# Optimization experiments

Measured on AMD Instinct MI355X. Metric: run time of the kernel, lower is better.

Reference implementation:

```python
import jax, jax.numpy as jnp
import numpy as np

B, S, MEM, L, E, H = 8, 512, 512, 4, 512, 8
DH = E // H
OBS = 128
K = MEM + S


def setup_inputs() -> dict:
    key = jax.random.key(0)
    ks = jax.random.split(key, 16)
    def w(k, shape, s=0.02):
        return jax.random.normal(k, shape, jnp.float32) * s
    # causal-with-memory mask: query i may attend to kv positions j <= MEM + i
    mask = jnp.arange(K)[None, None, None, :] <= (MEM + jnp.arange(S))[None, None, :, None]
    return {
        "obs": w(ks[0], (B, S, OBS), 1.0),
        "memories": w(ks[1], (B, MEM, L, E), 1.0),
        "mask": mask,
        "W_enc": w(ks[2], (OBS, E)), "b_enc": jnp.zeros((E,), jnp.float32),
        "ln1_s": jnp.ones((L, E), jnp.float32), "ln1_b": jnp.zeros((L, E), jnp.float32),
        "Wq": w(ks[3], (L, E, H, DH)), "bq": jnp.zeros((L, H, DH), jnp.float32),
        "Wk": w(ks[4], (L, E, H, DH)), "bk": jnp.zeros((L, H, DH), jnp.float32),
        "Wv": w(ks[5], (L, E, H, DH)), "bv": jnp.zeros((L, H, DH), jnp.float32),
        "Wr": w(ks[6], (L, E, H, DH)),
        "u_bias": w(ks[7], (L, H, DH)), "v_bias": w(ks[8], (L, H, DH)),
        "Wo": w(ks[9], (L, H, DH, E)), "bo": jnp.zeros((L, E), jnp.float32),
        "ln2_s": jnp.ones((L, E), jnp.float32), "ln2_b": jnp.zeros((L, E), jnp.float32),
        "W1": w(ks[10], (L, E, E)), "b1": jnp.zeros((L, E), jnp.float32),
        "W2": w(ks[11], (L, E, E)), "b2": jnp.zeros((L, E), jnp.float32),
    }


def _ln(x, s, b, eps=1e-6):
    m = x.mean(-1, keepdims=True)
    v = ((x - m) ** 2).mean(-1, keepdims=True)
    return (x - m) * jax.lax.rsqrt(v + eps) * s + b


def _rel_shift(x):
    # Transformer-XL relative shift: [B,H,Q,Kk] -> shifted [B,H,Q,Kk]
    b, h, q, k = x.shape
    x = jnp.pad(x, ((0, 0), (0, 0), (0, 0), (1, 0)))
    return x.reshape(b, h, k + 1, q)[:, :, 1:, :].reshape(b, h, q, k)


def _forward(obs, memories, mask, W_enc, b_enc, ln1_s, ln1_b, Wq, bq, Wk, bk, Wv, bv,
             Wr, u_bias, v_bias, Wo, bo, ln2_s, ln2_b, W1, b1, W2, b2):
    x = obs @ W_enc + b_enc  # [B,S,E]
    klen = memories.shape[1] + x.shape[1]
    e = x.shape[-1]
    # PositionalEmbedding: pos_seq = [klen, klen-1, ..., 1]
    inv_freq = 1.0 / (10000.0 ** (jnp.arange(0, e, 2, dtype=jnp.float32) / e))
    sin_inp = jnp.outer(jnp.arange(klen, 0, -1, dtype=jnp.float32), inv_freq)
    pe = jnp.concatenate([jnp.sin(sin_inp), jnp.cos(sin_inp)], axis=-1)  # [K,E]
    scale = 1.0 / jnp.sqrt(jnp.asarray(Wq.shape[-1], jnp.float32))
    for i in range(Wq.shape[0]):
        mem_cat = jnp.concatenate([memories[:, :, i], x], axis=1)  # [B,K,E]
        vk = _ln(mem_cat, ln1_s[i], ln1_b[i])
        qn = _ln(x, ln1_s[i], ln1_b[i])
        q = jnp.einsum('bse,ehd->bshd', qn, Wq[i]) + bq[i]
        k = jnp.einsum('bke,ehd->bkhd', vk, Wk[i]) + bk[i]
        vv = jnp.einsum('bke,ehd->bkhd', vk, Wv[i]) + bv[i]
        r = jnp.einsum('ke,ehd->khd', pe, Wr[i])
        ac = jnp.einsum('bqhd,bkhd->bhqk', q + u_bias[i], k)     # content term
        bd = _rel_shift(jnp.einsum('bqhd,khd->bhqk', q + v_bias[i], r))  # position term
        scores = jnp.where(mask, (ac + bd) * scale, jnp.float32(-1e30))
        attn = jax.nn.softmax(scores, axis=-1)
        o = jnp.einsum('bhqk,bkhd->bqhd', attn, vv)
        attn_out = jnp.einsum('bqhd,hde->bqe', o, Wo[i]) + bo[i]
        h = x + attn_out                      # residual (gating=False)
        hn = _ln(h, ln2_s[i], ln2_b[i])
        ff = jax.nn.gelu(hn @ W1[i] + b1[i]) @ W2[i] + b2[i]
        x = ff + h
    return x


def reference(obs, memories, mask, W_enc, b_enc, ln1_s, ln1_b, Wq, bq, Wk, bk, Wv, bv,
              Wr, u_bias, v_bias, Wo, bo, ln2_s, ln2_b, W1, b1, W2, b2):
    return _forward(obs, memories, mask, W_enc, b_enc, ln1_s, ln1_b, Wq, bq, Wk, bk,
                    Wv, bv, Wr, u_bias, v_bias, Wo, bo, ln2_s, ln2_b, W1, b1, W2, b2)
```

## Files before the change

kernel.cpp:

```cpp
#include <hip/hip_runtime.h>
#include <hip/hip_bf16.h>
#include <math.h>

#define B     8
#define S     512
#define MEM   512
#define L     4
#define E     512
#define H     8
#define DH    64
#define OBS   128
#define KLEN  1024
#define FQ    64
#define FK    64

typedef __hip_bfloat16 bf16;
using frag_ab = __attribute__((ext_vector_type(8))) short;
using frag_cd = __attribute__((ext_vector_type(4))) float;

__device__ __forceinline__ float gelu_tanh(float x) {
    return 0.5f * x * (1.0f + tanhf(0.7978845608028654f * (x + 0.044715f * x * x * x)));
}
__device__ __forceinline__ unsigned short f2bs(float x) {
    bf16 h = __float2bfloat16(x); return *(unsigned short*)&h;
}
__device__ __forceinline__ float bs2f(short s) {
    union { unsigned u; float f; } t; t.u = ((unsigned)(unsigned short)s) << 16; return t.f;
}

__global__ __launch_bounds__(256) void setup_kernel(
    const float* __restrict__ obs, bf16* __restrict__ obsb, bf16* __restrict__ pe)
{
    const int i = blockIdx.x * 256 + threadIdx.x;
    if (i < B * S * OBS) {
        obsb[i] = __float2bfloat16(obs[i]);
    } else {
        const int idx = i - B * S * OBS;
        const int p = idx >> 9;
        const int j = idx & 511;
        const float pos = (float)(KLEN - p);
        const int m = (j < 256) ? j : (j - 256);
        const float invf = expf(-(float)(2 * m) * (9.210340371976184f / (float)E));
        const float a = pos * invf;
        pe[idx] = __float2bfloat16((j < 256) ? sinf(a) : cosf(a));
    }
}

__global__ __launch_bounds__(256) void transpose_all_kernel(
    const float* __restrict__ Wq, const float* __restrict__ Wk,
    const float* __restrict__ Wv, const float* __restrict__ Wr,
    const float* __restrict__ Wo, const float* __restrict__ W1,
    const float* __restrict__ W2, const float* __restrict__ Wenc,
    bf16* __restrict__ WqT, bf16* __restrict__ WkvT, bf16* __restrict__ WrT,
    bf16* __restrict__ WoT, bf16* __restrict__ W1T, bf16* __restrict__ W2T,
    bf16* __restrict__ WencT)
{
    __shared__ float t[32][33];
    const int z = blockIdx.z;
    const int bn = blockIdx.x * 32, bk = blockIdx.y * 32;
    const int tx = threadIdx.x & 31, ty = threadIdx.x >> 5;
    if (z == 28) {
        if (blockIdx.y >= OBS / 32) return;
        #pragma unroll
        for (int r = 0; r < 32; r += 8)
            t[ty + r][tx] = Wenc[(size_t)(bk + ty + r) * E + bn + tx];
        __syncthreads();
        #pragma unroll
        for (int r = 0; r < 32; r += 8)
            WencT[(size_t)(bn + ty + r) * OBS + bk + tx] = __float2bfloat16(t[tx][ty + r]);
        return;
    }
    const int which = z >> 2, li = z & 3;
    const size_t so = (size_t)li * E * E;
    const float* src; bf16* dst;
    switch (which) {
        case 0: src = Wq + so; dst = WqT + so; break;
        case 1: src = Wk + so; dst = WkvT + (size_t)li * 2 * E * E; break;
        case 2: src = Wv + so; dst = WkvT + (size_t)li * 2 * E * E + (size_t)E * E; break;
        case 3: src = Wr + so; dst = WrT + so; break;
        case 4: src = Wo + so; dst = WoT + so; break;
        case 5: src = W1 + so; dst = W1T + so; break;
        default: src = W2 + so; dst = W2T + so; break;
    }
    #pragma unroll
    for (int r = 0; r < 32; r += 8)
        t[ty + r][tx] = src[(size_t)(bk + ty + r) * E + bn + tx];
    __syncthreads();
    #pragma unroll
    for (int r = 0; r < 32; r += 8)
        dst[(size_t)(bn + ty + r) * E + bk + tx] = __float2bfloat16(t[tx][ty + r]);
}

__global__ __launch_bounds__(256) void transpose_v_kernel(
    const bf16* __restrict__ Vn, bf16* __restrict__ Vt)
{
    __shared__ short ts[64][72];
    const int k0 = blockIdx.x * 64, d0 = blockIdx.y * 64, b = blockIdx.z;
    const int t = threadIdx.x;
    const int r = t >> 2, c = (t & 3) * 16;
    const short* src = (const short*)Vn + ((size_t)(b * KLEN + k0 + r)) * E + d0 + c;
    *(uint4*)&ts[r][c]     = *(const uint4*)(src);
    *(uint4*)&ts[r][c + 8] = *(const uint4*)(src + 8);
    __syncthreads();
    short vals[16];
    #pragma unroll
    for (int i = 0; i < 16; ++i) {
        const int kp = c + i;
        const int ks = ((kp & 3) << 4) | (kp >> 2);
        vals[i] = ts[ks][r];
    }
    short* dst = (short*)Vt + ((size_t)(b * E + d0 + r)) * KLEN + k0 + c;
    *(uint4*)(dst)     = *(const uint4*)&vals[0];
    *(uint4*)(dst + 8) = *(const uint4*)&vals[8];
}

__device__ __forceinline__ void gemm_body(
    short* As, short* Bs,
    const bf16* __restrict__ A, const bf16* __restrict__ Bt,
    int m0, int n0, int K, int N,
    const float* bias, const float* bias_u, const float* bias_v,
    const float* res, float* Cf, bf16* Cb, bf16* Cb2, int act, int mode)
{
    const int tid = threadIdx.x;
    const int w = tid >> 6, lane = tid & 63;
    const int wm2 = (w >> 1) * 64, wn2 = (w & 1) * 32;
    const int fr = lane & 15, quad = lane >> 4;

    const int arow = tid >> 1, acol = (tid & 1) * 32;
    const int brow = tid >> 2, bcol = (tid & 3) * 16;
    const short* Ag = (const short*)A + (size_t)(m0 + arow) * K + acol;
    const short* Bg = (const short*)Bt + (size_t)(n0 + brow) * K + bcol;
    short* Asw = &As[arow * 72 + acol];
    short* Bsw = &Bs[brow * 72 + bcol];

    frag_cd acc[4][2];
    #pragma unroll
    for (int i = 0; i < 4; ++i)
        #pragma unroll
        for (int j = 0; j < 2; ++j)
            acc[i][j] = (frag_cd)(0.0f);

    uint4 a0 = *(const uint4*)(Ag);
    uint4 a1 = *(const uint4*)(Ag + 8);
    uint4 a2 = *(const uint4*)(Ag + 16);
    uint4 a3 = *(const uint4*)(Ag + 24);
    uint4 b0 = *(const uint4*)(Bg);
    uint4 b1 = *(const uint4*)(Bg + 8);

    for (int k0 = 0; k0 < K; k0 += 64) {
        __syncthreads();
        *(uint4*)(Asw) = a0; *(uint4*)(Asw + 8) = a1;
        *(uint4*)(Asw + 16) = a2; *(uint4*)(Asw + 24) = a3;
        *(uint4*)(Bsw) = b0; *(uint4*)(Bsw + 8) = b1;
        if (k0 + 64 < K) {
            a0 = *(const uint4*)(Ag + k0 + 64);
            a1 = *(const uint4*)(Ag + k0 + 72);
            a2 = *(const uint4*)(Ag + k0 + 80);
            a3 = *(const uint4*)(Ag + k0 + 88);
            b0 = *(const uint4*)(Bg + k0 + 64);
            b1 = *(const uint4*)(Bg + k0 + 72);
        }
        asm volatile("s_waitcnt lgkmcnt(0)" ::: "memory");
        __builtin_amdgcn_s_barrier();
        __builtin_amdgcn_sched_barrier(0);
        #pragma unroll
        for (int kh = 0; kh < 2; ++kh) {
            frag_ab af[4], bfr[2];
            #pragma unroll
            for (int i = 0; i < 4; ++i)
                af[i] = *(const frag_ab*)&As[(wm2 + i * 16 + fr) * 72 + kh * 32 + quad * 8];
            #pragma unroll
            for (int j = 0; j < 2; ++j)
                bfr[j] = *(const frag_ab*)&Bs[(wn2 + j * 16 + fr) * 72 + kh * 32 + quad * 8];
            #pragma unroll
            for (int i = 0; i < 4; ++i)
                #pragma unroll
                for (int j = 0; j < 2; ++j)
                    acc[i][j] = __builtin_amdgcn_mfma_f32_16x16x32_bf16(af[i], bfr[j], acc[i][j], 0, 0, 0);
        }
    }

    #pragma unroll
    for (int i = 0; i < 4; ++i) {
        #pragma unroll
        for (int r = 0; r < 4; ++r) {
            const int m = m0 + wm2 + i * 16 + quad * 4 + r;
            #pragma unroll
            for (int j = 0; j < 2; ++j) {
                const int n = n0 + wn2 + j * 16 + fr;
                float v = acc[i][j][r];
                if (bias) v += bias[n];
                if (act)  v = gelu_tanh(v);
                if (res)  v += res[(size_t)m * N + n];
                if (mode == 2) {
                    if (n < 512) Cb[(size_t)m * 512 + n] = __float2bfloat16(v + bias_u[n]);
                    else Cb2[(size_t)m * 512 + (n - 512)] = __float2bfloat16(v + bias_v[n - 512]);
                } else if (mode == 1) {
                    Cb[(size_t)m * N + n]  = __float2bfloat16((v + bias_u[n]) * 0.125f);
                    Cb2[(size_t)m * N + n] = __float2bfloat16((v + bias_v[n]) * 0.125f);
                } else {
                    if (Cf) Cf[(size_t)m * N + n] = v;
                    if (Cb) Cb[(size_t)m * N + n] = __float2bfloat16(v);
                }
            }
        }
    }
}

__global__ __launch_bounds__(256) void mfma_gemm_kernel(
    const bf16* __restrict__ A, const bf16* __restrict__ Bt,
    const float* __restrict__ bias, const float* __restrict__ res,
    float* __restrict__ Cf, bf16* __restrict__ Cb,
    int K, int N, int act)
{
    __shared__ short As[128 * 72];
    __shared__ short Bs[64 * 72];
    const int pid = blockIdx.x;
    const int swz = ((pid & 7) << 5) | (pid >> 3);
    const int mblk = swz >> 3, nblk = swz & 7;
    gemm_body(As, Bs, A, Bt, mblk * 128, nblk * 64, K, N,
              bias, nullptr, nullptr, res, Cf, Cb, nullptr, act, 0);
}

__global__ __launch_bounds__(256) void qkvr_kernel(
    const bf16* __restrict__ QN, const bf16* __restrict__ VK,
    const bf16* __restrict__ PE_, const bf16* __restrict__ WqT,
    const bf16* __restrict__ WkvT, const bf16* __restrict__ WrT,
    const float* __restrict__ bq, const float* __restrict__ ub,
    const float* __restrict__ vbias, const float* __restrict__ bk,
    const float* __restrict__ bv,
    bf16* __restrict__ QU, bf16* __restrict__ QV,
    bf16* __restrict__ KB, bf16* __restrict__ VB, bf16* __restrict__ RB)
{
    __shared__ short As[128 * 72];
    __shared__ short Bs[64 * 72];
    const int bid = blockIdx.x;
    if (bid < 256) {
        const int swz = ((bid & 7) << 5) | (bid >> 3);
        gemm_body(As, Bs, QN, WqT, (swz >> 3) * 128, (swz & 7) * 64, E, E,
                  bq, ub, vbias, nullptr, nullptr, QU, QV, 0, 1);
    } else if (bid < 1280) {
        const int id = bid - 256;
        const int swz = ((id & 7) << 7) | (id >> 3);
        gemm_body(As, Bs, VK, WkvT, (swz >> 4) * 128, (swz & 15) * 64, E, 2 * E,
                  nullptr, bk, bv, nullptr, nullptr, KB, VB, 0, 2);
    } else {
        const int id = bid - 1280;
        const int swz = ((id & 7) << 3) | (id >> 3);
        gemm_body(As, Bs, PE_, WrT, (swz >> 3) * 128, (swz & 7) * 64, E, E,
                  nullptr, nullptr, nullptr, nullptr, nullptr, RB, nullptr, 0, 0);
    }
}

__global__ __launch_bounds__(256) void ln1_kernel(
    const float* __restrict__ mem, const float* __restrict__ X, int li,
    const float* __restrict__ gam, const float* __restrict__ bet,
    bf16* __restrict__ qn, bf16* __restrict__ vkdst)
{
    const int blk = blockIdx.x;
    const int t = threadIdx.x;
    const bool isMem = blk < B * MEM;
    const int rr = isMem ? blk : (blk - B * MEM);
    const float* sp = isMem ? (mem + ((size_t)rr * L + li) * E)
                            : (X + (size_t)rr * E);
    const float x0 = sp[t], x1 = sp[t + 256];
    float s = x0 + x1, ss = fmaf(x0, x0, x1 * x1);
    #pragma unroll
    for (int off = 32; off; off >>= 1) { s += __shfl_down(s, off, 64); ss += __shfl_down(ss, off, 64); }
    __shared__ float tmp[8];
    const int wid = t >> 6, lane = t & 63;
    if (!lane) { tmp[wid] = s; tmp[4 + wid] = ss; }
    __syncthreads();
    s = tmp[0] + tmp[1] + tmp[2] + tmp[3];
    ss = tmp[4] + tmp[5] + tmp[6] + tmp[7];
    const float mean = s * (1.0f / E);
    const float var = ss * (1.0f / E) - mean * mean;
    const float rstd = rsqrtf(var + 1e-6f);
    const float y0 = (x0 - mean) * rstd * gam[t] + bet[t];
    const float y1 = (x1 - mean) * rstd * gam[t + 256] + bet[t + 256];
    const int b = rr >> 9, p = rr & 511;
    if (isMem) {
        bf16* dst = vkdst + ((size_t)b * KLEN + p) * E;
        dst[t] = __float2bfloat16(y0); dst[t + 256] = __float2bfloat16(y1);
    } else {
        qn[(size_t)rr * E + t]       = __float2bfloat16(y0);
        qn[(size_t)rr * E + t + 256] = __float2bfloat16(y1);
        bf16* d2 = vkdst + ((size_t)b * KLEN + MEM + p) * E;
        d2[t] = __float2bfloat16(y0); d2[t + 256] = __float2bfloat16(y1);
    }
}

__global__ __launch_bounds__(256) void ln_f32_kernel(
    const float* __restrict__ src,
    const float* __restrict__ gam, const float* __restrict__ bet,
    bf16* __restrict__ dst1)
{
    const int rr = blockIdx.x;
    const int t = threadIdx.x;
    const float* sp = src + (size_t)rr * E;
    const float x0 = sp[t], x1 = sp[t + 256];
    float s = x0 + x1, ss = fmaf(x0, x0, x1 * x1);
    #pragma unroll
    for (int off = 32; off; off >>= 1) { s += __shfl_down(s, off, 64); ss += __shfl_down(ss, off, 64); }
    __shared__ float tmp[8];
    const int wid = t >> 6, lane = t & 63;
    if (!lane) { tmp[wid] = s; tmp[4 + wid] = ss; }
    __syncthreads();
    s = tmp[0] + tmp[1] + tmp[2] + tmp[3];
    ss = tmp[4] + tmp[5] + tmp[6] + tmp[7];
    const float mean = s * (1.0f / E);
    const float var = ss * (1.0f / E) - mean * mean;
    const float rstd = rsqrtf(var + 1e-6f);
    dst1[(size_t)rr * E + t]       = __float2bfloat16((x0 - mean) * rstd * gam[t] + bet[t]);
    dst1[(size_t)rr * E + t + 256] = __float2bfloat16((x1 - mean) * rstd * gam[t + 256] + bet[t + 256]);
}

__global__ __launch_bounds__(256) void mfma_flash_kernel(
    const bf16* __restrict__ Qu,
    const bf16* __restrict__ Qv,
    const bf16* __restrict__ Kb,
    const bf16* __restrict__ Vt,
    const bf16* __restrict__ Rb,
    bf16* __restrict__ O)
{
    const int pid = blockIdx.x;
    const int swz = ((pid & 7) << 6) | (pid >> 3);
    const int qphys = swz & 7;
    const int hb = swz >> 3;
    const int h = hb & 7, b = hb >> 3;
    const int qt = (qphys & 1) ? (7 - (qphys >> 1)) : (qphys >> 1);
    const int q0 = qt * FQ;
    const int t = threadIdx.x;
    const int w = t >> 6, lane = t & 63;
    const int fr = lane & 15, quad = lane >> 4;
    const int qbase = q0 + w * 16;

    __shared__ short Ks[64 * 64];
    __shared__ short Vs[64 * 64];
    __shared__ short Rs[128 * 64];
    __shared__ short BDs[4 * 80 * 18];
    __shared__ short Ps[4 * 16 * 64];

    const int fxk = fr & 7;
    const int xq0 = (quad ^ fxk) << 3;
    const int xq1 = ((quad + 4) ^ fxk) << 3;

    const short* quptr = (const short*)Qu + ((size_t)(b * S + qbase + fr)) * E + h * DH + quad * 8;
    const frag_ab au0 = *(const frag_ab*)(quptr);
    const frag_ab au1 = *(const frag_ab*)(quptr + 32);
    const short* qvptr = (const short*)Qv + ((size_t)(b * S + qbase + fr)) * E + h * DH + quad * 8;
    const frag_ab av0 = *(const frag_ab*)(qvptr);
    const frag_ab av1 = *(const frag_ab*)(qvptr + 32);

    frag_cd accO[4];
    #pragma unroll
    for (int i = 0; i < 4; ++i) accO[i] = (frag_cd)(0.0f);
    float mrow[4] = {-3.0e38f, -3.0e38f, -3.0e38f, -3.0e38f};
    float lrow[4] = {0.f, 0.f, 0.f, 0.f};

    const int srow = t >> 2, scol = (t & 3) * 16;
    const short* kg = (const short*)Kb + ((size_t)(b * KLEN + srow)) * E + h * DH + scol;
    const short* vg = (const short*)Vt + ((size_t)(b * E + h * DH + srow)) * KLEN + scol;
    const int sxs = srow & 7;
    const int scb = (t & 3) * 2;
    const int kvw0 = (srow << 6) + (((scb    ) ^ sxs) << 3);
    const int kvw1 = (srow << 6) + (((scb + 1) ^ sxs) << 3);
    const int ntb0 = 3 - w;
    const int b0 = 448 - q0;

    {
        const int rr = t >> 1, rc = (t & 1) * 32;
        const int j = b0 + rr;
        const int slot = j & 127;
        const int sx = slot & 7, cb = rc >> 3;
        const short* rp = (const short*)Rb + (size_t)j * E + h * DH + rc;
        *(uint4*)&Rs[(slot << 6) + (((cb    ) ^ sx) << 3)] = *(const uint4*)(rp);
        *(uint4*)&Rs[(slot << 6) + (((cb + 1) ^ sx) << 3)] = *(const uint4*)(rp + 8);
        *(uint4*)&Rs[(slot << 6) + (((cb + 2) ^ sx) << 3)] = *(const uint4*)(rp + 16);
        *(uint4*)&Rs[(slot << 6) + (((cb + 3) ^ sx) << 3)] = *(const uint4*)(rp + 24);
    }

    const int ntiles = 9 + qt;

    const int r64 = t >> 2, rc4 = (t & 3) * 16;
    uint4 ka0, ka1, va0, va1, ra0, ra1;
    int rslot = 0;
    {
        ka0 = *(const uint4*)(kg);
        ka1 = *(const uint4*)(kg + 8);
        va0 = *(const uint4*)(vg);
        va1 = *(const uint4*)(vg + 8);
    }

    for (int kt = 0; kt < ntiles; ++kt) {
        const int k0 = kt * FK;
        __syncthreads();
        {
            *(uint4*)&Ks[kvw0] = ka0;
            *(uint4*)&Ks[kvw1] = ka1;
            *(uint4*)&Vs[kvw0] = va0;
            *(uint4*)&Vs[kvw1] = va1;
        }
        if (kt >= 1) {
            const int sx = rslot & 7;
            *(uint4*)&Rs[(rslot << 6) + (((scb    ) ^ sx) << 3)] = ra0;
            *(uint4*)&Rs[(rslot << 6) + (((scb + 1) ^ sx) << 3)] = ra1;
        }
        if (kt + 1 < ntiles) {
            const short* kp = kg + (size_t)(k0 + FK) * E;
            ka0 = *(const uint4*)(kp);
            ka1 = *(const uint4*)(kp + 8);
            const short* vp = vg + k0 + FK;
            va0 = *(const uint4*)(vp);
            va1 = *(const uint4*)(vp + 8);
            int j = b0 + 64 * (kt + 1) + 64 + r64;
            rslot = j & 127;
            if (j > KLEN - 1) j = KLEN - 1;
            const short* rp = (const short*)Rb + (size_t)j * E + h * DH + rc4;
            ra0 = *(const uint4*)(rp);
            ra1 = *(const uint4*)(rp + 8);
        }
        asm volatile("s_waitcnt lgkmcnt(0)" ::: "memory");
        __builtin_amdgcn_s_barrier();
        __builtin_amdgcn_sched_barrier(0);

        const int roff = (b0 + 64 * kt) & 127;

        __builtin_amdgcn_s_setprio(1);
        #pragma unroll
        for (int i = 0; i < 5; ++i) {
            const int ntb = ntb0 + i;
            const int slot = (roff + ntb * 16 + fr) & 127;
            const frag_ab rf0 = *(const frag_ab*)&Rs[(slot << 6) + xq0];
            const frag_ab rf1 = *(const frag_ab*)&Rs[(slot << 6) + xq1];
            frag_cd z = (frag_cd)(0.0f);
            z = __builtin_amdgcn_mfma_f32_16x16x32_bf16(av0, rf0, z, 0, 0, 0);
            z = __builtin_amdgcn_mfma_f32_16x16x32_bf16(av1, rf1, z, 0, 0, 0);
            union { unsigned u[2]; unsigned short sh[4]; } pk;
            pk.sh[0] = f2bs(z[0]); pk.sh[1] = f2bs(z[1]);
            pk.sh[2] = f2bs(z[2]); pk.sh[3] = f2bs(z[3]);
            const int bdw = (w * 80 + i * 16 + fr) * 18 + quad * 4;
            *(unsigned*)&BDs[bdw]     = pk.u[0];
            *(unsigned*)&BDs[bdw + 2] = pk.u[1];
        }

        frag_cd sc[4];
        #pragma unroll
        for (int nt = 0; nt < 4; ++nt) {
            const int krow = (nt * 16 + fr) << 6;
            const frag_ab kf0 = *(const frag_ab*)&Ks[krow + xq0];
            const frag_ab kf1 = *(const frag_ab*)&Ks[krow + xq1];
            frag_cd z = (frag_cd)(0.0f);
            z = __builtin_amdgcn_mfma_f32_16x16x32_bf16(au0, kf0, z, 0, 0, 0);
            z = __builtin_amdgcn_mfma_f32_16x16x32_bf16(au1, kf1, z, 0, 0, 0);
            sc[nt] = z;
        }
        __builtin_amdgcn_s_setprio(0);

        const bool edge = (kt == ntiles - 1);
        #pragma unroll
        for (int r = 0; r < 4; ++r) {
            const int qw = quad * 4 + r;
            float sv[4];
            #pragma unroll
            for (int nt = 0; nt < 4; ++nt) {
                const int jlr = nt * 16 + fr + 15 - qw;
                const float bd = bs2f(BDs[(w * 80 + jlr) * 18 + qw]);
                sv[nt] = sc[nt][r] + bd;
            }
            if (edge) {
                const int qrow = qbase + qw;
                #pragma unroll
                for (int nt = 0; nt < 4; ++nt)
                    if (k0 + nt * 16 + fr > MEM + qrow) sv[nt] = -1e30f;
            }
            const float locmax = fmaxf(fmaxf(sv[0], sv[1]), fmaxf(sv[2], sv[3]));
            if (__any(locmax > mrow[r] + 4.0f)) {
                float tm = locmax;
                tm = fmaxf(tm, __shfl_xor(tm, 1, 64));
                tm = fmaxf(tm, __shfl_xor(tm, 2, 64));
                tm = fmaxf(tm, __shfl_xor(tm, 4, 64));
                tm = fmaxf(tm, __shfl_xor(tm, 8, 64));
                const float mn = fmaxf(mrow[r], tm);
                const float al = __expf(mrow[r] - mn);
                lrow[r] *= al;
                #pragma unroll
                for (int nt = 0; nt < 4; ++nt) accO[nt][r] *= al;
                mrow[r] = mn;
            }
            const float p0 = __expf(sv[0] - mrow[r]), p1 = __expf(sv[1] - mrow[r]);
            const float p2 = __expf(sv[2] - mrow[r]), p3 = __expf(sv[3] - mrow[r]);
            lrow[r] += (p0 + p1) + (p2 + p3);
            union { uint2 u2; unsigned short sh[4]; } pq;
            pq.sh[0] = f2bs(p0); pq.sh[1] = f2bs(p1);
            pq.sh[2] = f2bs(p2); pq.sh[3] = f2bs(p3);
            const int pw = (w << 10) + (qw << 6)
                         + (((fr >> 1) ^ (qw & 7)) << 3) + ((fr & 1) << 2);
            *(uint2*)&Ps[pw] = pq.u2;
        }

        const frag_ab pf0 = *(const frag_ab*)&Ps[(w << 10) + (fr << 6) + xq0];
        const frag_ab pf1 = *(const frag_ab*)&Ps[(w << 10) + (fr << 6) + xq1];
        __builtin_amdgcn_s_setprio(1);
        #pragma unroll
        for (int nt = 0; nt < 4; ++nt) {
            const int vrow = (nt * 16 + fr) << 6;
            const frag_ab vf0 = *(const frag_ab*)&Vs[vrow + xq0];
            const frag_ab vf1 = *(const frag_ab*)&Vs[vrow + xq1];
            accO[nt] = __builtin_amdgcn_mfma_f32_16x16x32_bf16(pf0, vf0, accO[nt], 0, 0, 0);
            accO[nt] = __builtin_amdgcn_mfma_f32_16x16x32_bf16(pf1, vf1, accO[nt], 0, 0, 0);
        }
        __builtin_amdgcn_s_setprio(0);
    }

    #pragma unroll
    for (int r = 0; r < 4; ++r) {
        float lsum = lrow[r];
        lsum += __shfl_xor(lsum, 1, 64);
        lsum += __shfl_xor(lsum, 2, 64);
        lsum += __shfl_xor(lsum, 4, 64);
        lsum += __shfl_xor(lsum, 8, 64);
        const float inv = 1.0f / lsum;
        bf16* po = O + ((size_t)(b * S + qbase + quad * 4 + r)) * E + h * DH + fr;
        #pragma unroll
        for (int nt = 0; nt < 4; ++nt)
            po[nt * 16] = __float2bfloat16(accO[nt][r] * inv);
    }
}

extern "C" void kernel_launch(void* const* d_in, const int* in_sizes, int n_in,
                              void* d_out, int out_size, void* d_ws, size_t ws_size,
                              hipStream_t stream)
{
    const float* obs  = (const float*)d_in[0];
    const float* mem  = (const float*)d_in[1];
    const float* Wenc = (const float*)d_in[3];
    const float* benc = (const float*)d_in[4];
    const float* ln1s = (const float*)d_in[5];
    const float* ln1b = (const float*)d_in[6];
    const float* Wq   = (const float*)d_in[7];
    const float* bq   = (const float*)d_in[8];
    const float* Wk   = (const float*)d_in[9];
    const float* bk   = (const float*)d_in[10];
    const float* Wv   = (const float*)d_in[11];
    const float* bv   = (const float*)d_in[12];
    const float* Wr   = (const float*)d_in[13];
    const float* ub   = (const float*)d_in[14];
    const float* vb   = (const float*)d_in[15];
    const float* Wo   = (const float*)d_in[16];
    const float* bo   = (const float*)d_in[17];
    const float* ln2s = (const float*)d_in[18];
    const float* ln2b = (const float*)d_in[19];
    const float* W1   = (const float*)d_in[20];
    const float* b1   = (const float*)d_in[21];
    const float* W2   = (const float*)d_in[22];
    const float* b2   = (const float*)d_in[23];

    float* wsf = (float*)d_ws;
    float* X = wsf;
    bf16* wsb = (bf16*)(wsf + (size_t)B * S * E);
    size_t ob = 0;
    bf16* OBSb = wsb + ob; ob += (size_t)B * S * OBS;
    bf16* QNb  = wsb + ob; ob += (size_t)B * S * E;
    bf16* PEb  = wsb + ob; ob += (size_t)KLEN * E;
    bf16* RBb  = wsb + ob; ob += (size_t)KLEN * E;
    bf16* WencT= wsb + ob; ob += (size_t)OBS * E;
    bf16* WqT  = wsb + ob; ob += (size_t)L * E * E;
    bf16* WkvT = wsb + ob; ob += (size_t)L * 2 * E * E;
    bf16* WrT  = wsb + ob; ob += (size_t)L * E * E;
    bf16* WoT  = wsb + ob; ob += (size_t)L * E * E;
    bf16* W1T  = wsb + ob; ob += (size_t)L * E * E;
    bf16* W2T  = wsb + ob; ob += (size_t)L * E * E;
    bf16* QUb  = wsb + ob; ob += (size_t)B * S * E;
    bf16* QVb  = wsb + ob; ob += (size_t)B * S * E;
    bf16* KBb  = wsb + ob; ob += (size_t)B * KLEN * E;
    bf16* VTb  = wsb + ob; ob += (size_t)B * E * KLEN;
    bf16* OBb  = wsb + ob; ob += (size_t)B * S * E;
    char* uni = (char*)(wsb + ob);
    bf16*  VKb = (bf16*)uni;
    bf16*  VBb = (bf16*)(uni + ((size_t)8 << 20));
    float* HB  = (float*)uni;
    bf16*  FFb = (bf16*)(uni + ((size_t)8 << 20));

    transpose_all_kernel<<<dim3(E / 32, E / 32, 29), 256, 0, stream>>>(
        Wq, Wk, Wv, Wr, Wo, W1, W2, Wenc, WqT, WkvT, WrT, WoT, W1T, W2T, WencT);
    setup_kernel<<<(B * S * OBS + KLEN * E) / 256, 256, 0, stream>>>(obs, OBSb, PEb);

    mfma_gemm_kernel<<<256, 256, 0, stream>>>(
        OBSb, WencT, benc, nullptr, X, nullptr, OBS, E, 0);

    for (int li = 0; li < L; ++li) {
        const size_t wOff = (size_t)li * E * E;
        const size_t vOff = (size_t)li * E;

        ln1_kernel<<<2 * B * S, 256, 0, stream>>>(
            mem, X, li, ln1s + vOff, ln1b + vOff, QNb, VKb);

        qkvr_kernel<<<1344, 256, 0, stream>>>(
            QNb, VKb, PEb, WqT + wOff, WkvT + (size_t)li * 2 * E * E, WrT + wOff,
            bq + vOff, ub + vOff, vb + vOff, bk + vOff, bv + vOff,
            QUb, QVb, KBb, VBb, RBb);

        transpose_v_kernel<<<dim3(KLEN / 64, E / 64, B), 256, 0, stream>>>(VBb, VTb);

        mfma_flash_kernel<<<512, 256, 0, stream>>>(
            QUb, QVb, KBb, VTb, RBb, OBb);

        mfma_gemm_kernel<<<256, 256, 0, stream>>>(
            OBb, WoT + wOff, bo + vOff, X, HB, nullptr, E, E, 0);
        ln_f32_kernel<<<B * S, 256, 0, stream>>>(HB, ln2s + vOff, ln2b + vOff, QNb);
        mfma_gemm_kernel<<<256, 256, 0, stream>>>(
            QNb, W1T + wOff, b1 + vOff, nullptr, nullptr, FFb, E, E, 1);
        mfma_gemm_kernel<<<256, 256, 0, stream>>>(
            FFb, W2T + wOff, b2 + vOff, HB, X, nullptr, E, E, 0);
    }

    hipMemcpyAsync(d_out, X, (size_t)B * S * E * sizeof(float),
                   hipMemcpyDeviceToDevice, stream);
}
```

Measured before the change: 702.6 us.

## Use direct global-to-LDS loads with XOR swizzle and double buffering in GEMM

Replaces the register-staged tile loads in the shared GEMM body with global_load_lds direct-to-LDS transfers into double-buffered shared tiles. Padding is replaced by an XOR swizzle to avoid bank conflicts. The next tile is prefetched while the current one is computed. This removes the register round trip and one barrier per iteration, at the cost of double the LDS footprint, which may lower occupancy.

```diff
diff --git a/kernel.cpp b/kernel.cpp
--- a/kernel.cpp
+++ b/kernel.cpp
@@ -26,6 +26,11 @@
 }
 __device__ __forceinline__ float bs2f(short s) {
     union { unsigned u; float f; } t; t.u = ((unsigned)(unsigned short)s) << 16; return t.f;
+}
+__device__ __forceinline__ void gload16(const short* g, short* l) {
+    __builtin_amdgcn_global_load_lds(
+        (const __attribute__((address_space(1))) void*)g,
+        (__attribute__((address_space(3))) void*)l, 16, 0, 0);
 }
 
 __global__ __launch_bounds__(256) void setup_kernel(
@@ -125,13 +130,16 @@
     const int w = tid >> 6, lane = tid & 63;
     const int wm2 = (w >> 1) * 64, wn2 = (w & 1) * 32;
     const int fr = lane & 15, quad = lane >> 4;
-
-    const int arow = tid >> 1, acol = (tid & 1) * 32;
-    const int brow = tid >> 2, bcol = (tid & 3) * 16;
-    const short* Ag = (const short*)A + (size_t)(m0 + arow) * K + acol;
-    const short* Bg = (const short*)Bt + (size_t)(n0 + brow) * K + bcol;
-    short* Asw = &As[arow * 72 + acol];
-    short* Bsw = &Bs[brow * 72 + bcol];
+    const int l3 = lane >> 3, l7 = lane & 7;
+    const int gch = (l7 ^ l3) * 8;
+
+    const size_t Kz = (size_t)K;
+    const short* Ag0 = (const short*)A + (size_t)(m0 + w * 32 + l3) * Kz + gch;
+    const short* Bg0 = (const short*)Bt + (size_t)(n0 + w * 16 + l3) * Kz + gch;
+
+    const int fx = fr & 7;
+    const int xq0 = (quad ^ fx) << 3;
+    const int xq1 = ((quad + 4) ^ fx) << 3;
 
     frag_cd acc[4][2];
     #pragma unroll
@@ -140,38 +148,42 @@
         for (int j = 0; j < 2; ++j)
             acc[i][j] = (frag_cd)(0.0f);
 
-    uint4 a0 = *(const uint4*)(Ag);
-    uint4 a1 = *(const uint4*)(Ag + 8);
-    uint4 a2 = *(const uint4*)(Ag + 16);
-    uint4 a3 = *(const uint4*)(Ag + 24);
-    uint4 b0 = *(const uint4*)(Bg);
-    uint4 b1 = *(const uint4*)(Bg + 8);
-
-    for (int k0 = 0; k0 < K; k0 += 64) {
-        __syncthreads();
-        *(uint4*)(Asw) = a0; *(uint4*)(Asw + 8) = a1;
-        *(uint4*)(Asw + 16) = a2; *(uint4*)(Asw + 24) = a3;
-        *(uint4*)(Bsw) = b0; *(uint4*)(Bsw + 8) = b1;
-        if (k0 + 64 < K) {
-            a0 = *(const uint4*)(Ag + k0 + 64);
-            a1 = *(const uint4*)(Ag + k0 + 72);
-            a2 = *(const uint4*)(Ag + k0 + 80);
-            a3 = *(const uint4*)(Ag + k0 + 88);
-            b0 = *(const uint4*)(Bg + k0 + 64);
-            b1 = *(const uint4*)(Bg + k0 + 72);
-        }
-        asm volatile("s_waitcnt lgkmcnt(0)" ::: "memory");
+    #pragma unroll
+    for (int i = 0; i < 4; ++i)
+        gload16(Ag0 + (size_t)(i * 8) * Kz, As + w * 2048 + i * 512);
+    #pragma unroll
+    for (int i = 0; i < 2; ++i)
+        gload16(Bg0 + (size_t)(i * 8) * Kz, Bs + w * 1024 + i * 512);
+
+    const int T = K >> 6;
+    for (int t = 0; t < T; ++t) {
+        const int cur = t & 1;
+        asm volatile("s_waitcnt vmcnt(0)" ::: "memory");
         __builtin_amdgcn_s_barrier();
         __builtin_amdgcn_sched_barrier(0);
+        if (t + 1 < T) {
+            const int nb = cur ^ 1;
+            const int k0 = (t + 1) << 6;
+            #pragma unroll
+            for (int i = 0; i < 4; ++i)
+                gload16(Ag0 + (size_t)(i * 8) * Kz + k0, As + nb * 8192 + w * 2048 + i * 512);
+            #pragma unroll
+            for (int i = 0; i < 2; ++i)
+                gload16(Bg0 + (size_t)(i * 8) * Kz + k0, Bs + nb * 4096 + w * 1024 + i * 512);
+        }
+        __builtin_amdgcn_sched_barrier(0);
+        const short* Ab = As + cur * 8192;
+        const short* Bb = Bs + cur * 4096;
         #pragma unroll
         for (int kh = 0; kh < 2; ++kh) {
+            const int xq = kh ? xq1 : xq0;
             frag_ab af[4], bfr[2];
             #pragma unroll
             for (int i = 0; i < 4; ++i)
-                af[i] = *(const frag_ab*)&As[(wm2 + i * 16 + fr) * 72 + kh * 32 + quad * 8];
+                af[i] = *(const frag_ab*)&Ab[(wm2 + i * 16 + fr) * 64 + xq];
             #pragma unroll
             for (int j = 0; j < 2; ++j)
-                bfr[j] = *(const frag_ab*)&Bs[(wn2 + j * 16 + fr) * 72 + kh * 32 + quad * 8];
+                bfr[j] = *(const frag_ab*)&Bb[(wn2 + j * 16 + fr) * 64 + xq];
             #pragma unroll
             for (int i = 0; i < 4; ++i)
                 #pragma unroll
@@ -213,8 +225,8 @@
     float* __restrict__ Cf, bf16* __restrict__ Cb,
     int K, int N, int act)
 {
-    __shared__ short As[128 * 72];
-    __shared__ short Bs[64 * 72];
+    __shared__ short As[2 * 128 * 64];
+    __shared__ short Bs[2 * 64 * 64];
     const int pid = blockIdx.x;
     const int swz = ((pid & 7) << 5) | (pid >> 3);
     const int mblk = swz >> 3, nblk = swz & 7;
@@ -232,8 +244,8 @@
     bf16* __restrict__ QU, bf16* __restrict__ QV,
     bf16* __restrict__ KB, bf16* __restrict__ VB, bf16* __restrict__ RB)
 {
-    __shared__ short As[128 * 72];
-    __shared__ short Bs[64 * 72];
+    __shared__ short As[2 * 128 * 64];
+    __shared__ short Bs[2 * 64 * 64];
     const int bid = blockIdx.x;
     if (bid < 256) {
         const int swz = ((bid & 7) << 5) | (bid >> 3);
```

Measured after the change: 724.8 us. +3.2%, slower.

## Use 64x64 GEMM tiles with 512 blocks and write final output directly

Applied to the files above, without the earlier changes.

Replaces the 128x64-tile GEMM body used by the dense projection GEMMs with a new 64x64-tile body, doubling the grid to 512 blocks. The goal is better CU occupancy on a 4096x512 problem, since 256 blocks underfill the device. The last layer's W2 GEMM now writes straight into the output buffer, which drops the final device-to-device memcpy. Smaller tiles lower data reuse per block and raise global load traffic.

```diff
diff --git a/kernel.cpp b/kernel.cpp
--- a/kernel.cpp
+++ b/kernel.cpp
@@ -207,19 +207,96 @@
     }
 }
 
+__device__ __forceinline__ void gemm64_body(
+    short* As, short* Bs,
+    const bf16* __restrict__ A, const bf16* __restrict__ Bt,
+    int m0, int n0, int K, int N,
+    const float* bias, const float* res, float* Cf, bf16* Cb, int act)
+{
+    const int tid = threadIdx.x;
+    const int w = tid >> 6, lane = tid & 63;
+    const int wm2 = (w >> 1) * 32, wn2 = (w & 1) * 32;
+    const int fr = lane & 15, quad = lane >> 4;
+
+    const int arow = tid >> 2, acol = (tid & 3) * 16;
+    const short* Ag = (const short*)A + (size_t)(m0 + arow) * K + acol;
+    const short* Bg = (const short*)Bt + (size_t)(n0 + arow) * K + acol;
+    short* Asw = &As[arow * 72 + acol];
+    short* Bsw = &Bs[arow * 72 + acol];
+
+    frag_cd acc[2][2];
+    #pragma unroll
+    for (int i = 0; i < 2; ++i)
+        #pragma unroll
+        for (int j = 0; j < 2; ++j)
+            acc[i][j] = (frag_cd)(0.0f);
+
+    uint4 a0 = *(const uint4*)(Ag);
+    uint4 a1 = *(const uint4*)(Ag + 8);
+    uint4 b0 = *(const uint4*)(Bg);
+    uint4 b1 = *(const uint4*)(Bg + 8);
+
+    for (int k0 = 0; k0 < K; k0 += 64) {
+        __syncthreads();
+        *(uint4*)(Asw) = a0; *(uint4*)(Asw + 8) = a1;
+        *(uint4*)(Bsw) = b0; *(uint4*)(Bsw + 8) = b1;
+        if (k0 + 64 < K) {
+            a0 = *(const uint4*)(Ag + k0 + 64);
+            a1 = *(const uint4*)(Ag + k0 + 72);
+            b0 = *(const uint4*)(Bg + k0 + 64);
+            b1 = *(const uint4*)(Bg + k0 + 72);
+        }
+        asm volatile("s_waitcnt lgkmcnt(0)" ::: "memory");
+        __builtin_amdgcn_s_barrier();
+        __builtin_amdgcn_sched_barrier(0);
+        #pragma unroll
+        for (int kh = 0; kh < 2; ++kh) {
+            frag_ab af[2], bfr[2];
+            #pragma unroll
+            for (int i = 0; i < 2; ++i)
+                af[i] = *(const frag_ab*)&As[(wm2 + i * 16 + fr) * 72 + kh * 32 + quad * 8];
+            #pragma unroll
+            for (int j = 0; j < 2; ++j)
+                bfr[j] = *(const frag_ab*)&Bs[(wn2 + j * 16 + fr) * 72 + kh * 32 + quad * 8];
+            #pragma unroll
+            for (int i = 0; i < 2; ++i)
+                #pragma unroll
+                for (int j = 0; j < 2; ++j)
+                    acc[i][j] = __builtin_amdgcn_mfma_f32_16x16x32_bf16(af[i], bfr[j], acc[i][j], 0, 0, 0);
+        }
+    }
+
+    #pragma unroll
+    for (int i = 0; i < 2; ++i) {
+        #pragma unroll
+        for (int r = 0; r < 4; ++r) {
+            const int m = m0 + wm2 + i * 16 + quad * 4 + r;
+            #pragma unroll
+            for (int j = 0; j < 2; ++j) {
+                const int n = n0 + wn2 + j * 16 + fr;
+                float v = acc[i][j][r];
+                if (bias) v += bias[n];
+                if (act)  v = gelu_tanh(v);
+                if (res)  v += res[(size_t)m * N + n];
+                if (Cf) Cf[(size_t)m * N + n] = v;
+                if (Cb) Cb[(size_t)m * N + n] = __float2bfloat16(v);
+            }
+        }
+    }
+}
+
 __global__ __launch_bounds__(256) void mfma_gemm_kernel(
     const bf16* __restrict__ A, const bf16* __restrict__ Bt,
     const float* __restrict__ bias, const float* __restrict__ res,
     float* __restrict__ Cf, bf16* __restrict__ Cb,
     int K, int N, int act)
 {
-    __shared__ short As[128 * 72];
+    __shared__ short As[64 * 72];
     __shared__ short Bs[64 * 72];
     const int pid = blockIdx.x;
-    const int swz = ((pid & 7) << 5) | (pid >> 3);
-    const int mblk = swz >> 3, nblk = swz & 7;
-    gemm_body(As, Bs, A, Bt, mblk * 128, nblk * 64, K, N,
-              bias, nullptr, nullptr, res, Cf, Cb, nullptr, act, 0);
+    const int swz = ((pid & 7) << 6) | (pid >> 3);
+    gemm64_body(As, Bs, A, Bt, (swz >> 3) * 64, (swz & 7) * 64, K, N,
+                bias, res, Cf, Cb, act);
 }
 
 __global__ __launch_bounds__(256) void qkvr_kernel(
@@ -586,7 +663,7 @@
         Wq, Wk, Wv, Wr, Wo, W1, W2, Wenc, WqT, WkvT, WrT, WoT, W1T, W2T, WencT);
     setup_kernel<<<(B * S * OBS + KLEN * E) / 256, 256, 0, stream>>>(obs, OBSb, PEb);
 
-    mfma_gemm_kernel<<<256, 256, 0, stream>>>(
+    mfma_gemm_kernel<<<512, 256, 0, stream>>>(
         OBSb, WencT, benc, nullptr, X, nullptr, OBS, E, 0);
 
     for (int li = 0; li < L; ++li) {
@@ -606,15 +683,13 @@
         mfma_flash_kernel<<<512, 256, 0, stream>>>(
             QUb, QVb, KBb, VTb, RBb, OBb);
 
-        mfma_gemm_kernel<<<256, 256, 0, stream>>>(
+        mfma_gemm_kernel<<<512, 256, 0, stream>>>(
             OBb, WoT + wOff, bo + vOff, X, HB, nullptr, E, E, 0);
         ln_f32_kernel<<<B * S, 256, 0, stream>>>(HB, ln2s + vOff, ln2b + vOff, QNb);
-        mfma_gemm_kernel<<<256, 256, 0, stream>>>(
+        mfma_gemm_kernel<<<512, 256, 0, stream>>>(
             QNb, W1T + wOff, b1 + vOff, nullptr, nullptr, FFb, E, E, 1);
-        mfma_gemm_kernel<<<256, 256, 0, stream>>>(
-            FFb, W2T + wOff, b2 + vOff, HB, X, nullptr, E, E, 0);
-    }
-
-    hipMemcpyAsync(d_out, X, (size_t)B * S * E * sizeof(float),
-                   hipMemcpyDeviceToDevice, stream);
-}
+        float* dst = (li == L - 1) ? (float*)d_out : X;
+        mfma_gemm_kernel<<<512, 256, 0, stream>>>(
+            FFb, W2T + wOff, b2 + vOff, HB, dst, nullptr, E, E, 0);
+    }
+}
```

Result: faster. 624.8 us (-11.1%).
